# Optimization experiments

Measured on AMD Instinct MI355X. Metric: run time of the kernel, lower is better.

Reference implementation:

```python
import jax, jax.numpy as jnp
import numpy as np

H = 4096
IN = 512
OUT = 64


def setup_inputs() -> dict:
    key = jax.random.key(0)
    ks = jax.random.split(key, 10)
    return {
        "inp": jax.random.normal(ks[0], (1, IN), jnp.float32),
        "hidden": jax.random.normal(ks[1], (1, H), jnp.float32),
        "hebb": jax.random.normal(ks[2], (H, H), jnp.float32) * 0.01,
        "W_i2h": jax.random.normal(ks[3], (H, IN), jnp.float32) * (1.0 / np.sqrt(IN)),
        "b_i2h": jax.random.normal(ks[4], (H,), jnp.float32),
        "w": jax.random.uniform(ks[5], (H, H), jnp.float32) * 0.01,
        "plas": jax.random.uniform(ks[6], (H, H), jnp.float32) * 0.01,
        "learn": jnp.full((1,), 0.01, jnp.float32),
        "W_h2o": jax.random.normal(ks[7], (OUT, H), jnp.float32) * (1.0 / np.sqrt(H)),
        "b_h2o": jax.random.normal(ks[8], (OUT,), jnp.float32),
    }


def reference(inp, hidden, hebb, W_i2h, b_i2h, w, plas, learn, W_h2o, b_h2o):
    # plastic-Miconi, rule='hebb', activ='relu'
    # x = relu(i2h(input) + hidden @ (w + plas * hebb))   [1, H]
    pre = inp @ W_i2h.T + b_i2h + hidden @ (w + plas * hebb)
    x = jax.nn.relu(pre)
    # hebb <- (1 - learn) * hebb + learn * outer(hidden, x)   [H, H]
    hebb_new = (1.0 - learn) * hebb + learn * (hidden.T @ x)
    # output = tanh(h2o(x))   [1, OUT]
    out = jnp.tanh(x @ W_h2o.T + b_h2o)
    return out, x, hebb_new
```

## Files before the change

kernel.cpp:

```cpp
#include <hip/hip_runtime.h>
#include <math.h>

#define H 4096
#define INP 512
#define OUTN 64
#define H4 (H / 4)
#define SPLITS 512
#define RPS (H / SPLITS)

typedef float fx4 __attribute__((ext_vector_type(4)));

__global__ __launch_bounds__(256) void k_partial(
    const float* __restrict__ hidden,
    const float* __restrict__ w,
    const float* __restrict__ plas,
    const float* __restrict__ hebb,
    float* __restrict__ partial)
{
    const int col4 = blockIdx.x * 256 + threadIdx.x;
    const int i0   = blockIdx.y * RPS;
    const fx4* __restrict__ w4 = (const fx4*)w;
    const fx4* __restrict__ p4 = (const fx4*)plas;
    const fx4* __restrict__ h4 = (const fx4*)hebb;
    const size_t base = (size_t)i0 * H4 + col4;

    float hv[RPS];
#pragma unroll
    for (int r = 0; r < RPS; ++r)
        hv[r] = hidden[i0 + r];

    fx4 hb[RPS], wv[RPS], pv[RPS];
#pragma unroll
    for (int r = 0; r < RPS; ++r) {
        const size_t idx = base + (size_t)r * H4;
        hb[r] = h4[idx];
        wv[r] = __builtin_nontemporal_load(w4 + idx);
        pv[r] = __builtin_nontemporal_load(p4 + idx);
    }
    __builtin_amdgcn_sched_barrier(0);

    fx4 acc = (fx4)(0.f);
#pragma unroll
    for (int r = 0; r < RPS; ++r)
        acc += hv[r] * (wv[r] + pv[r] * hb[r]);

    ((fx4*)partial)[(size_t)blockIdx.y * H4 + col4] = acc;
}

__global__ __launch_bounds__(1024) void k_reduce_x(
    const float* __restrict__ partial,
    const float* __restrict__ inp,
    const float* __restrict__ W_i2h,
    const float* __restrict__ b_i2h,
    float* __restrict__ x_out)
{
    const int jl  = threadIdx.x & 31;
    const int grp = threadIdx.x >> 5;
    const int j   = blockIdx.x * 32 + jl;

    float ps[SPLITS / 32];
    const float* __restrict__ p = partial + (size_t)grp * (SPLITS / 32) * H + j;
#pragma unroll
    for (int s = 0; s < SPLITS / 32; ++s)
        ps[s] = p[(size_t)s * H];
    __builtin_amdgcn_sched_barrier(0);

    float sum = 0.f;
#pragma unroll
    for (int s = 0; s < SPLITS / 32; ++s)
        sum += ps[s];

    const fx4* __restrict__ row4 = (const fx4*)(W_i2h + (size_t)j * INP);
    const fx4* __restrict__ in4  = (const fx4*)inp;
#pragma unroll
    for (int c = 0; c < 4; ++c) {
        const fx4 a = row4[grp * 4 + c];
        const fx4 b = in4[grp * 4 + c];
        sum += a.x * b.x + a.y * b.y + a.z * b.z + a.w * b.w;
    }

    __shared__ float red[32][33];
    red[grp][jl] = sum;
    __syncthreads();
    if (threadIdx.x < 32) {
        float t = 0.f;
#pragma unroll
        for (int g = 0; g < 32; ++g) t += red[g][jl];
        const float pre = t + b_i2h[j];
        x_out[j] = pre > 0.f ? pre : 0.f;
    }
}

__global__ __launch_bounds__(256) void k_tail(
    const float* __restrict__ hebb,
    const float* __restrict__ hidden,
    const float* __restrict__ x,
    const float* __restrict__ learn,
    const float* __restrict__ W_h2o,
    const float* __restrict__ b_h2o,
    float* __restrict__ hebb_out,
    float* __restrict__ out)
{
    if (blockIdx.x < H) {
        const int i = blockIdx.x;
        const float lr   = learn[0];
        const float om   = 1.f - lr;
        const float coef = lr * hidden[i];
        const fx4* __restrict__ hb4 = (const fx4*)hebb + (size_t)i * H4;
        const fx4* __restrict__ xx4 = (const fx4*)x;
        fx4* __restrict__ o4 = (fx4*)hebb_out + (size_t)i * H4;

        const int t = threadIdx.x;
        fx4 a[4], xv[4];
#pragma unroll
        for (int q = 0; q < 4; ++q) {
            a[q]  = hb4[t + q * 256];
            xv[q] = xx4[t + q * 256];
        }
        __builtin_amdgcn_sched_barrier(0);
#pragma unroll
        for (int q = 0; q < 4; ++q)
            __builtin_nontemporal_store(om * a[q] + coef * xv[q], o4 + t + q * 256);
    } else {
        const int o = blockIdx.x - H;
        const fx4* __restrict__ row4 = (const fx4*)(W_h2o + (size_t)o * H);
        const fx4* __restrict__ x4   = (const fx4*)x;
        float sum = 0.f;
#pragma unroll
        for (int c = threadIdx.x; c < H4; c += 256) {
            const fx4 a = row4[c];
            const fx4 b = x4[c];
            sum += a.x * b.x + a.y * b.y + a.z * b.z + a.w * b.w;
        }
#pragma unroll
        for (int off = 32; off > 0; off >>= 1)
            sum += __shfl_down(sum, off, 64);
        __shared__ float red[4];
        const int lane = threadIdx.x & 63;
        const int wave = threadIdx.x >> 6;
        if (lane == 0) red[wave] = sum;
        __syncthreads();
        if (threadIdx.x == 0) {
            const float s = red[0] + red[1] + red[2] + red[3];
            out[o] = tanhf(s + b_h2o[o]);
        }
    }
}

extern "C" void kernel_launch(void* const* d_in, const int* in_sizes, int n_in,
                              void* d_out, int out_size, void* d_ws, size_t ws_size,
                              hipStream_t stream)
{
    const float* inp    = (const float*)d_in[0];
    const float* hidden = (const float*)d_in[1];
    const float* hebb   = (const float*)d_in[2];
    const float* W_i2h  = (const float*)d_in[3];
    const float* b_i2h  = (const float*)d_in[4];
    const float* w      = (const float*)d_in[5];
    const float* plas   = (const float*)d_in[6];
    const float* learn  = (const float*)d_in[7];
    const float* W_h2o  = (const float*)d_in[8];
    const float* b_h2o  = (const float*)d_in[9];

    float* out      = (float*)d_out;
    float* x        = out + OUTN;
    float* hebb_out = x + H;

    const size_t part_bytes = (size_t)SPLITS * H * sizeof(float);
    float* partial = (ws_size >= part_bytes) ? (float*)d_ws : hebb_out;

    k_partial<<<dim3(H4 / 256, SPLITS), 256, 0, stream>>>(hidden, w, plas, hebb, partial);
    k_reduce_x<<<H / 32, 1024, 0, stream>>>(partial, inp, W_i2h, b_i2h, x);
    k_tail<<<H + OUTN, 256, 0, stream>>>(hebb, hidden, x, learn, W_h2o, b_h2o, hebb_out, out);
}
```

Before: 239.6 us.

## Remap partial GEMV to full-row blocks with double-buffered register staging

The partial mat-vec kernel now uses one block per group of 4 rows, with each thread covering 4 column vectors. Loads of w, plas and hebb are software-pipelined through two register buffers, separated by scheduling barriers, so memory fetches overlap with the FMAs. The number of splits doubles from 512 to 1024, so the partial buffer written and then re-read by the reduction kernel also doubles in size. That extra traffic may offset the gain from better memory-level parallelism.

```diff
diff --git a/kernel.cpp b/kernel.cpp
--- a/kernel.cpp
+++ b/kernel.cpp
@@ -5,7 +5,7 @@
 #define INP 512
 #define OUTN 64
 #define H4 (H / 4)
-#define SPLITS 512
+#define SPLITS 1024
 #define RPS (H / SPLITS)
 
 typedef float fx4 __attribute__((ext_vector_type(4)));
@@ -17,34 +17,58 @@
     const float* __restrict__ hebb,
     float* __restrict__ partial)
 {
-    const int col4 = blockIdx.x * 256 + threadIdx.x;
-    const int i0   = blockIdx.y * RPS;
+    const int t  = threadIdx.x;
+    const int s  = blockIdx.x;
+    const int i0 = s * RPS;
     const fx4* __restrict__ w4 = (const fx4*)w;
     const fx4* __restrict__ p4 = (const fx4*)plas;
     const fx4* __restrict__ h4 = (const fx4*)hebb;
-    const size_t base = (size_t)i0 * H4 + col4;
 
-    float hv[RPS];
+    const float hv0 = hidden[i0 + 0];
+    const float hv1 = hidden[i0 + 1];
+    const float hv2 = hidden[i0 + 2];
+    const float hv3 = hidden[i0 + 3];
+
+    fx4 hbA[4], wvA[4], pvA[4];
+    fx4 hbB[4], wvB[4], pvB[4];
+    fx4 acc[4];
 #pragma unroll
-    for (int r = 0; r < RPS; ++r)
-        hv[r] = hidden[i0 + r];
+    for (int q = 0; q < 4; ++q) acc[q] = (fx4)(0.f);
 
-    fx4 hb[RPS], wv[RPS], pv[RPS];
+    const size_t r0 = (size_t)i0 * H4 + t;
+
+#define STAGE(dsth, dstw, dstp, row)                                   \
+    _Pragma("unroll")                                                  \
+    for (int q = 0; q < 4; ++q) {                                      \
+        const size_t idx = r0 + (size_t)(row) * H4 + q * 256;          \
+        dsth[q] = h4[idx];                                             \
+        dstw[q] = __builtin_nontemporal_load(w4 + idx);                \
+        dstp[q] = __builtin_nontemporal_load(p4 + idx);                \
+    }
+
+#define COMPUTE(hb, wv, pv, hv)                                        \
+    _Pragma("unroll")                                                  \
+    for (int q = 0; q < 4; ++q)                                        \
+        acc[q] += (hv) * (wv[q] + pv[q] * hb[q]);
+
+    STAGE(hbA, wvA, pvA, 0)
+    STAGE(hbB, wvB, pvB, 1)
+    __builtin_amdgcn_sched_barrier(0);
+    COMPUTE(hbA, wvA, pvA, hv0)
+    STAGE(hbA, wvA, pvA, 2)
+    __builtin_amdgcn_sched_barrier(0);
+    COMPUTE(hbB, wvB, pvB, hv1)
+    STAGE(hbB, wvB, pvB, 3)
+    __builtin_amdgcn_sched_barrier(0);
+    COMPUTE(hbA, wvA, pvA, hv2)
+    COMPUTE(hbB, wvB, pvB, hv3)
+#undef STAGE
+#undef COMPUTE
+
+    fx4* __restrict__ o4 = (fx4*)partial + (size_t)s * H4 + t;
 #pragma unroll
-    for (int r = 0; r < RPS; ++r) {
-        const size_t idx = base + (size_t)r * H4;
-        hb[r] = h4[idx];
-        wv[r] = __builtin_nontemporal_load(w4 + idx);
-        pv[r] = __builtin_nontemporal_load(p4 + idx);
-    }
-    __builtin_amdgcn_sched_barrier(0);
-
-    fx4 acc = (fx4)(0.f);
-#pragma unroll
-    for (int r = 0; r < RPS; ++r)
-        acc += hv[r] * (wv[r] + pv[r] * hb[r]);
-
-    ((fx4*)partial)[(size_t)blockIdx.y * H4 + col4] = acc;
+    for (int q = 0; q < 4; ++q)
+        o4[q * 256] = acc[q];
 }
 
 __global__ __launch_bounds__(1024) void k_reduce_x(
@@ -58,17 +82,11 @@
     const int grp = threadIdx.x >> 5;
     const int j   = blockIdx.x * 32 + jl;
 
-    float ps[SPLITS / 32];
+    float sum = 0.f;
     const float* __restrict__ p = partial + (size_t)grp * (SPLITS / 32) * H + j;
 #pragma unroll
     for (int s = 0; s < SPLITS / 32; ++s)
-        ps[s] = p[(size_t)s * H];
-    __builtin_amdgcn_sched_barrier(0);
-
-    float sum = 0.f;
-#pragma unroll
-    for (int s = 0; s < SPLITS / 32; ++s)
-        sum += ps[s];
+        sum += p[(size_t)s * H];
 
     const fx4* __restrict__ row4 = (const fx4*)(W_i2h + (size_t)j * INP);
     const fx4* __restrict__ in4  = (const fx4*)inp;
@@ -83,10 +101,10 @@
     red[grp][jl] = sum;
     __syncthreads();
     if (threadIdx.x < 32) {
-        float t = 0.f;
+        float tsum = 0.f;
 #pragma unroll
-        for (int g = 0; g < 32; ++g) t += red[g][jl];
-        const float pre = t + b_i2h[j];
+        for (int g = 0; g < 32; ++g) tsum += red[g][jl];
+        const float pre = tsum + b_i2h[j];
         x_out[j] = pre > 0.f ? pre : 0.f;
     }
 }
@@ -141,8 +159,8 @@
         if (lane == 0) red[wave] = sum;
         __syncthreads();
         if (threadIdx.x == 0) {
-            const float s = red[0] + red[1] + red[2] + red[3];
-            out[o] = tanhf(s + b_h2o[o]);
+            const float ssum = red[0] + red[1] + red[2] + red[3];
+            out[o] = tanhf(ssum + b_h2o[o]);
         }
     }
 }
@@ -169,7 +187,7 @@
     const size_t part_bytes = (size_t)SPLITS * H * sizeof(float);
     float* partial = (ws_size >= part_bytes) ? (float*)d_ws : hebb_out;
 
-    k_partial<<<dim3(H4 / 256, SPLITS), 256, 0, stream>>>(hidden, w, plas, hebb, partial);
+    k_partial<<<SPLITS, 256, 0, stream>>>(hidden, w, plas, hebb, partial);
     k_reduce_x<<<H / 32, 1024, 0, stream>>>(partial, inp, W_i2h, b_i2h, x);
     k_tail<<<H + OUTN, 256, 0, stream>>>(hebb, hidden, x, learn, W_h2o, b_h2o, hebb_out, out);
 }
```

New measurement: 246.4 us. 1.03x slower.
